# Performance work log

Measured on AMD Instinct MI355X. Metric: run time of the kernel, lower is better.

## Reference

```python
import jax, jax.numpy as jnp
import numpy as np

# Unpooled output spatial size (pooled 128x128 -> unpooled 256x256)
OUT_H, OUT_W = 256, 256


def setup_inputs() -> dict:
    key = jax.random.key(0)
    k1, k2, k3, k4 = jax.random.split(key, 4)
    B, C, OH, OW = 16, 64, 128, 128
    K, P = 4, 4  # kernel_size samples, bilinear taps
    x = jax.random.normal(k1, (B, C, OH, OW), dtype=jnp.float32)
    idx_mask = jax.random.randint(k2, (B, C, OH, OW), 0, K, dtype=jnp.int64)
    sample_map = jax.random.randint(k3, (OH, OW, K, P), 0, OUT_H * OUT_W, dtype=jnp.int64)
    interp_weights = jax.random.uniform(k4, (OH, OW, K, P), dtype=jnp.float32)
    return {"x": x, "idx_mask": idx_mask, "sample_map": sample_map,
            "interp_weights": interp_weights}


def reference(x, idx_mask, sample_map, interp_weights):
    # x: (B,C,OH,OW) pooled values; idx_mask: (B,C,OH,OW) argmax kernel sample in [0,K)
    # sample_map: (OH,OW,K,P) flat indices into OUT_H*OUT_W; interp_weights: (OH,OW,K,P)
    B, C, OH, OW = x.shape
    P = sample_map.shape[-1]
    oh = jnp.arange(OH)[:, None]
    ow = jnp.arange(OW)[None, :]
    # Select, per (b,c,oh,ow), the winning kernel sample's taps and weights -> (B,C,OH,OW,P)
    sel_idx = sample_map[oh, ow, idx_mask]
    sel_w = interp_weights[oh, ow, idx_mask]
    vals = sel_w * x[..., None]  # (B,C,OH,OW,P)
    bb = jnp.arange(B)[:, None, None, None, None]
    cc = jnp.arange(C)[None, :, None, None, None]
    out = jnp.zeros((B, C, OUT_H * OUT_W), dtype=x.dtype)
    out = out.at[bb, cc, sel_idx].add(vals)  # scatter-add (atomic add in CUDA kernel)
    return out.reshape(B, C, OUT_H, OUT_W)
```

## Files before the change

### kernel.cpp

```cpp
#include <hip/hip_runtime.h>
#include <hip/hip_fp16.h>

constexpr int B  = 16;
constexpr int C  = 64;
constexpr int OH = 128;
constexpr int OW = 128;
constexpr int HW = OH * OW;
constexpr int K  = 4;
constexpr int P  = 4;
constexpr int TAPS = HW * K * P;
constexpr int OUT_H = 256;
constexpr int OUT_W = 256;
constexpr int PLANE = OUT_H * OUT_W;
constexpr int NQ = 4;
constexpr int QUARTER = PLANE / NQ;
constexpr int BLOCK = 512;
constexpr size_t TABLE_BYTES = (size_t)HW * K * 16;

constexpr int CHUNK_CAP = 114688;
constexpr size_t WS_SORT_BYTES = ((size_t)PLANE * 5) * 4 + (size_t)CHUNK_CAP * 16;

constexpr int GW = 4;

static __device__ __forceinline__ float h2f(unsigned short u) {
    __half h; __builtin_memcpy(&h, &u, 2); return __half2float(h);
}


__global__ __launch_bounds__(256) void zero_ws_kernel(
    unsigned* __restrict__ counts, uint4* __restrict__ entries)
{
    int r = blockIdx.x * 256 + threadIdx.x;
    if (r < PLANE)     counts[r]  = 0u;
    if (r < CHUNK_CAP) entries[r] = make_uint4(0u, 0u, 0u, 0u);
}

__global__ __launch_bounds__(256) void hist_kernel(
    const int* __restrict__ sm, unsigned* __restrict__ counts)
{
    int r = blockIdx.x * 256 + threadIdx.x;
    if (r < TAPS) atomicAdd(&counts[sm[r]], 1u);
}

__global__ __launch_bounds__(1024) void scan_chunks_kernel(
    const unsigned* __restrict__ counts,
    unsigned* __restrict__ desc, unsigned* __restrict__ cursor)
{
    __shared__ unsigned part[1024];
    const int t = threadIdx.x;
    const int base = t * 64;
    unsigned s = 0;
    for (int j = 0; j < 64; ++j) s += (counts[base + j] + 3u) >> 2;
    part[t] = s;
    __syncthreads();
    for (int st = 1; st < 1024; st <<= 1) {
        unsigned v = (t >= st) ? part[t - st] : 0u;
        __syncthreads();
        part[t] += v;
        __syncthreads();
    }
    unsigned run = part[t] - s;
    for (int j = 0; j < 64; ++j) {
        unsigned c   = counts[base + j];
        unsigned nch = (c + 3u) >> 2;
        desc[base + j]   = run | (nch << 24);
        cursor[base + j] = run * 4u;
        run += nch;
    }
}

__global__ __launch_bounds__(256) void scatter_chunks_kernel(
    const int* __restrict__ sm, const float* __restrict__ iw,
    unsigned* __restrict__ cursor, unsigned* __restrict__ entries_u32)
{
    int r = blockIdx.x * 256 + threadIdx.x;
    if (r >= TAPS) return;
    int o = sm[r];
    unsigned hw = (unsigned)(r >> 4);
    unsigned k  = (unsigned)((r >> 2) & 3);
    __half h = __float2half_rn(iw[r]);
    unsigned short hb; __builtin_memcpy(&hb, &h, 2);
    unsigned ent = (hw << 2) | k | ((unsigned)hb << 16);
    unsigned pos = atomicAdd(&cursor[o], 1u);
    entries_u32[pos] = ent;
}

constexpr int WNB = 32;
__global__ __launch_bounds__(256) void window_sort_kernel(
    const unsigned* __restrict__ desc, uint2* __restrict__ sched)
{
    __shared__ unsigned hist[WNB];
    __shared__ unsigned cur[WNB];
    const int w = blockIdx.x;
    const int t = threadIdx.x;
    const int base = w * 1024;
    if (t < WNB) hist[t] = 0;
    __syncthreads();
    unsigned d[4], nch[4];
    for (int j = 0; j < 4; ++j) {
        d[j] = desc[base + t * 4 + j];
        nch[j] = d[j] >> 24; if (nch[j] > 31u) nch[j] = 31u;
        atomicAdd(&hist[nch[j]], 1u);
    }
    __syncthreads();
    if (t == 0) {
        unsigned run = 0;
        for (int b = 0; b < WNB; ++b) { unsigned v = hist[b]; cur[b] = run; run += v; }
    }
    __syncthreads();
    for (int j = 0; j < 4; ++j) {
        unsigned p = atomicAdd(&cur[nch[j]], 1u);
        sched[base + p] = make_uint2(d[j], (unsigned)(base + t * 4 + j));
    }
}

__global__ __launch_bounds__(1024) void unpool_staged_kernel(
    const float* __restrict__ x,
    const int*   __restrict__ idx_mask,
    const uint2* __restrict__ sched,
    const uint4* __restrict__ entries,
    float* __restrict__ out)
{
    __shared__ unsigned xk[HW];
    __shared__ float    stg[GW * 1024];

    const int bc = blockIdx.x;
    const float4* xp4 = (const float4*)(x + (size_t)bc * HW);
    const int4*   ip4 = (const int4*)(idx_mask + (size_t)bc * HW);
    uint4* xk4 = (uint4*)xk;

    for (int t = threadIdx.x; t < HW / 4; t += 1024) {
        float4 xv = xp4[t];
        int4   kv = ip4[t];
        uint4 o;
        o.x = (__float_as_uint(xv.x) & ~3u) | ((unsigned)kv.x & 3u);
        o.y = (__float_as_uint(xv.y) & ~3u) | ((unsigned)kv.y & 3u);
        o.z = (__float_as_uint(xv.z) & ~3u) | ((unsigned)kv.z & 3u);
        o.w = (__float_as_uint(xv.w) & ~3u) | ((unsigned)kv.w & 3u);
        xk4[t] = o;
    }
    __syncthreads();

    const char* xkb = (const char*)xk;
    const float4* stg4 = (const float4*)stg;
    float4* op4 = (float4*)(out + (size_t)bc * PLANE);

    const int lane = threadIdx.x & 63;
    const int wid  = threadIdx.x >> 6;

    for (int g = 0; g < PLANE / 1024 / GW; ++g) {
        for (int iw2 = 0; iw2 < GW; ++iw2) {
            const int i = g * GW + iw2;
            const int slot = i * 1024 + (((wid + i) & 15) << 6) + lane;
            const uint2 s = sched[slot];
            const unsigned nch = s.x >> 24;
            const uint4* ep = entries + (s.x & 0xffffffu);
            float acc = 0.f;
            for (unsigned j = 0; j < nch; ++j) {
                uint4 ch = ep[j];
                {   unsigned e = ch.x;
                    unsigned u = *(const unsigned*)(xkb + (e & 0xfffcu));
                    float w = (((u ^ e) & 3u) == 0u) ? h2f((unsigned short)(e >> 16)) : 0.f;
                    acc = fmaf(w, __uint_as_float(u & ~3u), acc); }
                {   unsigned e = ch.y;
                    unsigned u = *(const unsigned*)(xkb + (e & 0xfffcu));
                    float w = (((u ^ e) & 3u) == 0u) ? h2f((unsigned short)(e >> 16)) : 0.f;
                    acc = fmaf(w, __uint_as_float(u & ~3u), acc); }
                {   unsigned e = ch.z;
                    unsigned u = *(const unsigned*)(xkb + (e & 0xfffcu));
                    float w = (((u ^ e) & 3u) == 0u) ? h2f((unsigned short)(e >> 16)) : 0.f;
                    acc = fmaf(w, __uint_as_float(u & ~3u), acc); }
                {   unsigned e = ch.w;
                    unsigned u = *(const unsigned*)(xkb + (e & 0xfffcu));
                    float w = (((u ^ e) & 3u) == 0u) ? h2f((unsigned short)(e >> 16)) : 0.f;
                    acc = fmaf(w, __uint_as_float(u & ~3u), acc); }
            }
            stg[iw2 * 1024 + (s.y & 1023)] = acc;
        }
        __syncthreads();
        op4[g * 1024 + threadIdx.x] = stg4[threadIdx.x];
        __syncthreads();
    }
}

__global__ __launch_bounds__(1024) void unpool_chunk_kernel(
    const float* __restrict__ x,
    const int*   __restrict__ idx_mask,
    const unsigned* __restrict__ desc,
    const uint4* __restrict__ entries,
    float* __restrict__ out)
{
    __shared__ unsigned xk[HW];

    const int bc = blockIdx.x;
    const float4* xp4 = (const float4*)(x + (size_t)bc * HW);
    const int4*   ip4 = (const int4*)(idx_mask + (size_t)bc * HW);
    uint4* xk4 = (uint4*)xk;

    for (int t = threadIdx.x; t < HW / 4; t += 1024) {
        float4 xv = xp4[t];
        int4   kv = ip4[t];
        uint4 o;
        o.x = (__float_as_uint(xv.x) & ~3u) | ((unsigned)kv.x & 3u);
        o.y = (__float_as_uint(xv.y) & ~3u) | ((unsigned)kv.y & 3u);
        o.z = (__float_as_uint(xv.z) & ~3u) | ((unsigned)kv.z & 3u);
        o.w = (__float_as_uint(xv.w) & ~3u) | ((unsigned)kv.w & 3u);
        xk4[t] = o;
    }
    __syncthreads();

    const char* xkb = (const char*)xk;
    float* op = out + (size_t)bc * PLANE;

    for (int i = 0; i < PLANE / 1024; ++i) {
        const int o = i * 1024 + threadIdx.x;
        const unsigned d   = desc[o];
        const unsigned nch = d >> 24;
        const uint4* ep = entries + (d & 0xffffffu);
        float acc = 0.f;
        for (unsigned j = 0; j < nch; ++j) {
            uint4 ch = ep[j];
            {   unsigned e = ch.x;
                unsigned u = *(const unsigned*)(xkb + (e & 0xfffcu));
                float w = (((u ^ e) & 3u) == 0u) ? h2f((unsigned short)(e >> 16)) : 0.f;
                acc = fmaf(w, __uint_as_float(u & ~3u), acc); }
            {   unsigned e = ch.y;
                unsigned u = *(const unsigned*)(xkb + (e & 0xfffcu));
                float w = (((u ^ e) & 3u) == 0u) ? h2f((unsigned short)(e >> 16)) : 0.f;
                acc = fmaf(w, __uint_as_float(u & ~3u), acc); }
            {   unsigned e = ch.z;
                unsigned u = *(const unsigned*)(xkb + (e & 0xfffcu));
                float w = (((u ^ e) & 3u) == 0u) ? h2f((unsigned short)(e >> 16)) : 0.f;
                acc = fmaf(w, __uint_as_float(u & ~3u), acc); }
            {   unsigned e = ch.w;
                unsigned u = *(const unsigned*)(xkb + (e & 0xfffcu));
                float w = (((u ^ e) & 3u) == 0u) ? h2f((unsigned short)(e >> 16)) : 0.f;
                acc = fmaf(w, __uint_as_float(u & ~3u), acc); }
        }
        op[o] = acc;
    }
}


static __device__ __forceinline__ uint4 sel4(bool c, uint4 a, uint4 b) {
    return make_uint4(c ? a.x : b.x, c ? a.y : b.y, c ? a.z : b.z, c ? a.w : b.w);
}
static __device__ __forceinline__ float2 u2f2(unsigned u) {
    __half2 h; __builtin_memcpy(&h, &u, 4); return __half22float2(h);
}

__global__ __launch_bounds__(256) void compact_table_kernel(
    const int4* __restrict__ sm, const float4* __restrict__ iw, uint4* __restrict__ ct)
{
    int r = blockIdx.x * blockDim.x + threadIdx.x;
    if (r >= HW * K) return;
    int4   s = sm[r];
    float4 w = iw[r];
    uint4 o;
    o.x = ((unsigned)s.x & 0xffffu) | (((unsigned)s.y & 0xffffu) << 16);
    o.y = ((unsigned)s.z & 0xffffu) | (((unsigned)s.w & 0xffffu) << 16);
    __half2 h01 = __floats2half2_rn(w.x, w.y);
    __half2 h23 = __floats2half2_rn(w.z, w.w);
    __builtin_memcpy(&o.z, &h01, 4);
    __builtin_memcpy(&o.w, &h23, 4);
    ct[r] = o;
}

__global__ __launch_bounds__(BLOCK) void unpool_lds2_kernel(
    const float* __restrict__ x,
    const int*   __restrict__ idx_mask,
    const uint4* __restrict__ ct,
    float* __restrict__ out)
{
    __shared__ float acc[QUARTER];

    const int bc    = blockIdx.x >> 2;
    const int q     = blockIdx.x & 3;
    const int qbase = q * QUARTER;

    float4* acc4 = (float4*)acc;
    for (int t = threadIdx.x; t < QUARTER / 4; t += BLOCK)
        acc4[t] = make_float4(0.f, 0.f, 0.f, 0.f);
    __syncthreads();

    const float* xp = x + (size_t)bc * HW;
    const int*   ip = idx_mask + (size_t)bc * HW;

    for (int hw = threadIdx.x; hw < HW; hw += BLOCK) {
        float xv = xp[hw];
        int   k  = ip[hw];
        const uint4* c = ct + (hw << 2);
        uint4 r0 = c[0], r1 = c[1], r2 = c[2], r3 = c[3];
        uint4 rl = sel4(k & 1, r1, r0);
        uint4 rh = sel4(k & 1, r3, r2);
        uint4 r  = sel4(k & 2, rh, rl);

        int i0 = r.x & 0xffff, i1 = (int)(r.x >> 16);
        int i2 = r.y & 0xffff, i3 = (int)(r.y >> 16);
        float2 w01 = u2f2(r.z);
        float2 w23 = u2f2(r.w);

        int a;
        a = i0 - qbase; if ((unsigned)a < (unsigned)QUARTER) atomicAdd(&acc[a], w01.x * xv);
        a = i1 - qbase; if ((unsigned)a < (unsigned)QUARTER) atomicAdd(&acc[a], w01.y * xv);
        a = i2 - qbase; if ((unsigned)a < (unsigned)QUARTER) atomicAdd(&acc[a], w23.x * xv);
        a = i3 - qbase; if ((unsigned)a < (unsigned)QUARTER) atomicAdd(&acc[a], w23.y * xv);
    }
    __syncthreads();

    float4* op4 = (float4*)(out + (size_t)bc * PLANE + qbase);
    for (int t = threadIdx.x; t < QUARTER / 4; t += BLOCK)
        op4[t] = acc4[t];
}

__global__ __launch_bounds__(256) void unpool_lds_fallback_kernel(
    const float* __restrict__ x,
    const int*   __restrict__ idx_mask,
    const int4*  __restrict__ sample_map,
    const float4* __restrict__ interp_w,
    float* __restrict__ out)
{
    __shared__ float acc[QUARTER];
    const int bc    = blockIdx.x >> 2;
    const int q     = blockIdx.x & 3;
    const int qbase = q * QUARTER;
    float4* acc4 = (float4*)acc;
    for (int t = threadIdx.x; t < QUARTER / 4; t += 256)
        acc4[t] = make_float4(0.f, 0.f, 0.f, 0.f);
    __syncthreads();
    const float* xp = x + (size_t)bc * HW;
    const int*   ip = idx_mask + (size_t)bc * HW;
    for (int hw = threadIdx.x; hw < HW; hw += 256) {
        float xv = xp[hw];
        int   k  = ip[hw];
        int row = hw * K + k;
        int4   sel = sample_map[row];
        float4 w   = interp_w[row];
        int a;
        a = sel.x - qbase; if ((unsigned)a < (unsigned)QUARTER) atomicAdd(&acc[a], w.x * xv);
        a = sel.y - qbase; if ((unsigned)a < (unsigned)QUARTER) atomicAdd(&acc[a], w.y * xv);
        a = sel.z - qbase; if ((unsigned)a < (unsigned)QUARTER) atomicAdd(&acc[a], w.z * xv);
        a = sel.w - qbase; if ((unsigned)a < (unsigned)QUARTER) atomicAdd(&acc[a], w.w * xv);
    }
    __syncthreads();
    float4* op4 = (float4*)(out + (size_t)bc * PLANE + qbase);
    for (int t = threadIdx.x; t < QUARTER / 4; t += 256)
        op4[t] = acc4[t];
}

extern "C" void kernel_launch(void* const* d_in, const int* in_sizes, int n_in,
                              void* d_out, int out_size, void* d_ws, size_t ws_size,
                              hipStream_t stream) {
    const float*  x          = (const float*)d_in[0];
    const int*    idx_mask   = (const int*)d_in[1];
    const int*    sample_map = (const int*)d_in[2];
    const float*  interp_w   = (const float*)d_in[3];
    float* out = (float*)d_out;

    if (ws_size >= WS_SORT_BYTES) {
        unsigned* desc    = (unsigned*)d_ws;
        unsigned* cursor  = desc + PLANE;
        unsigned* counts  = cursor + PLANE;
        uint2*    sched   = (uint2*)(counts + PLANE);
        uint4*    entries = (uint4*)(counts + PLANE + 2 * PLANE);

        zero_ws_kernel<<<(CHUNK_CAP + 255) / 256, 256, 0, stream>>>(counts, entries);
        hist_kernel<<<TAPS / 256, 256, 0, stream>>>(sample_map, counts);
        scan_chunks_kernel<<<1, 1024, 0, stream>>>(counts, desc, cursor);
        scatter_chunks_kernel<<<TAPS / 256, 256, 0, stream>>>(
            sample_map, interp_w, cursor, (unsigned*)entries);
        window_sort_kernel<<<PLANE / 1024, 256, 0, stream>>>(desc, sched);
        unpool_staged_kernel<<<B * C, 1024, 0, stream>>>(x, idx_mask, sched, entries, out);
        if (hipGetLastError() != hipSuccess) {
            unpool_chunk_kernel<<<B * C, 1024, 0, stream>>>(x, idx_mask, desc, entries, out);
        }
    } else if (ws_size >= TABLE_BYTES) {
        uint4* ct = (uint4*)d_ws;
        compact_table_kernel<<<(HW * K + 255) / 256, 256, 0, stream>>>(
            (const int4*)sample_map, (const float4*)interp_w, ct);
        unpool_lds2_kernel<<<B * C * NQ, BLOCK, 0, stream>>>(
            x, idx_mask, ct, out);
    } else {
        unpool_lds_fallback_kernel<<<B * C * NQ, 256, 0, stream>>>(
            x, idx_mask, (const int4*)sample_map, (const float4*)interp_w, out);
    }
}
```

Baseline: 546.6 us.

## Interleave per-group tap entries for coalesced wavefront loads in unpool gather

Adds a new workspace path that groups output pixels into 64-wide groups sorted by chunk count, then lays out their tap entries interleaved by lane so each wavefront reads contiguous uint4s per step. A group scan computes per-group base offsets and the scatter kernel writes entries into the strided interleaved layout. The gather kernel prefetches the next chunk and stages results in LDS for coalesced output stores. It needs a larger workspace and pads every group to its longest member's chunk count, which adds wasted entries. The old chunk fallback kernel is removed.

```diff
diff --git a/kernel.cpp b/kernel.cpp
--- a/kernel.cpp
+++ b/kernel.cpp
@@ -17,13 +17,172 @@
 constexpr int BLOCK = 512;
 constexpr size_t TABLE_BYTES = (size_t)HW * K * 16;
 
+constexpr int GW = 4;
+constexpr int NGROUP = PLANE / 64;
+
+constexpr int E2CAP = 229376;
+constexpr size_t WS_V2_BYTES = ((size_t)PLANE * 4 + 2048) * 4 + (size_t)E2CAP * 16;
+
 constexpr int CHUNK_CAP = 114688;
 constexpr size_t WS_SORT_BYTES = ((size_t)PLANE * 5) * 4 + (size_t)CHUNK_CAP * 16;
 
-constexpr int GW = 4;
-
 static __device__ __forceinline__ float h2f(unsigned short u) {
     __half h; __builtin_memcpy(&h, &u, 2); return __half2float(h);
+}
+
+
+__global__ __launch_bounds__(256) void hist_kernel(
+    const int* __restrict__ sm, unsigned* __restrict__ counts)
+{
+    int r = blockIdx.x * 256 + threadIdx.x;
+    if (r < TAPS) atomicAdd(&counts[sm[r]], 1u);
+}
+
+
+__global__ __launch_bounds__(256) void zero_v2_kernel(
+    unsigned* __restrict__ counts, unsigned* __restrict__ cursor,
+    uint4* __restrict__ entries2)
+{
+    int r = blockIdx.x * 256 + threadIdx.x;
+    if (r < PLANE) { counts[r] = 0u; cursor[r] = 0u; }
+    if (r < E2CAP) entries2[r] = make_uint4(0u, 0u, 0u, 0u);
+}
+
+constexpr int WNB = 32;
+__global__ __launch_bounds__(256) void window_sort_v2_kernel(
+    const unsigned* __restrict__ counts, unsigned* __restrict__ sched)
+{
+    __shared__ unsigned hist[WNB];
+    __shared__ unsigned cur[WNB];
+    const int w = blockIdx.x;
+    const int t = threadIdx.x;
+    const int base = w * 1024;
+    if (t < WNB) hist[t] = 0;
+    __syncthreads();
+    unsigned nch[4];
+    for (int j = 0; j < 4; ++j) {
+        unsigned c = counts[base + t * 4 + j];
+        nch[j] = (c + 3u) >> 2; if (nch[j] > 31u) nch[j] = 31u;
+        atomicAdd(&hist[nch[j]], 1u);
+    }
+    __syncthreads();
+    if (t == 0) {
+        unsigned run = 0;
+        for (int b = 0; b < WNB; ++b) { unsigned v = hist[b]; cur[b] = run; run += v; }
+    }
+    __syncthreads();
+    for (int j = 0; j < 4; ++j) {
+        unsigned p = atomicAdd(&cur[nch[j]], 1u);
+        sched[base + p] = (unsigned)(base + t * 4 + j);
+    }
+}
+
+__global__ __launch_bounds__(1024) void group_scan_kernel(
+    const unsigned* __restrict__ counts, const unsigned* __restrict__ sched,
+    unsigned* __restrict__ gdesc, unsigned* __restrict__ wbase)
+{
+    __shared__ unsigned part[NGROUP];
+    const int g = threadIdx.x;
+    unsigned olast = sched[g * 64 + 63];
+    unsigned M = (counts[olast] + 3u) >> 2;
+    part[g] = M;
+    __syncthreads();
+    for (int st = 1; st < NGROUP; st <<= 1) {
+        unsigned v = (g >= st) ? part[g - st] : 0u;
+        __syncthreads();
+        part[g] += v;
+        __syncthreads();
+    }
+    unsigned rowbase = part[g] - M;
+    gdesc[g] = (rowbase << 6) | (M << 24);
+    unsigned wb = (rowbase << 6) * 4u;
+    for (int l = 0; l < 64; ++l)
+        wbase[sched[g * 64 + l]] = wb + (unsigned)(l * 4);
+}
+
+__global__ __launch_bounds__(256) void scatter_v2_kernel(
+    const int* __restrict__ sm, const float* __restrict__ iw,
+    unsigned* __restrict__ cursor, const unsigned* __restrict__ wbase,
+    unsigned* __restrict__ entries2_u32)
+{
+    int r = blockIdx.x * 256 + threadIdx.x;
+    if (r >= TAPS) return;
+    int o = sm[r];
+    unsigned hw = (unsigned)(r >> 4);
+    unsigned k  = (unsigned)((r >> 2) & 3);
+    __half h = __float2half_rn(iw[r]);
+    unsigned short hb; __builtin_memcpy(&hb, &h, 2);
+    unsigned ent = (hw << 2) | k | ((unsigned)hb << 16);
+    unsigned idx = atomicAdd(&cursor[o], 1u);
+    entries2_u32[wbase[o] + ((idx >> 2) << 8) + (idx & 3u)] = ent;
+}
+
+__global__ __launch_bounds__(1024) void unpool_grouped_kernel(
+    const float* __restrict__ x,
+    const int*   __restrict__ idx_mask,
+    const unsigned* __restrict__ sched,
+    const unsigned* __restrict__ gdesc,
+    const uint4* __restrict__ entries2,
+    float* __restrict__ out)
+{
+    __shared__ unsigned xk[HW];
+    __shared__ float    stg[GW * 1024];
+
+    const int bc = blockIdx.x;
+    const float4* xp4 = (const float4*)(x + (size_t)bc * HW);
+    const int4*   ip4 = (const int4*)(idx_mask + (size_t)bc * HW);
+    uint4* xk4 = (uint4*)xk;
+
+    for (int t = threadIdx.x; t < HW / 4; t += 1024) {
+        float4 xv = xp4[t];
+        int4   kv = ip4[t];
+        uint4 o;
+        o.x = (__float_as_uint(xv.x) & ~3u) | ((unsigned)kv.x & 3u);
+        o.y = (__float_as_uint(xv.y) & ~3u) | ((unsigned)kv.y & 3u);
+        o.z = (__float_as_uint(xv.z) & ~3u) | ((unsigned)kv.z & 3u);
+        o.w = (__float_as_uint(xv.w) & ~3u) | ((unsigned)kv.w & 3u);
+        xk4[t] = o;
+    }
+    __syncthreads();
+
+    const char* xkb = (const char*)xk;
+    const float4* stg4 = (const float4*)stg;
+    float4* op4 = (float4*)(out + (size_t)bc * PLANE);
+
+    const int lane = threadIdx.x & 63;
+    const int wid  = threadIdx.x >> 6;
+
+#define PROC1(E) { unsigned e = (E); \
+    unsigned u = *(const unsigned*)(xkb + (e & 0xfffcu)); \
+    float w = (((u ^ e) & 3u) == 0u) ? h2f((unsigned short)(e >> 16)) : 0.f; \
+    acc = fmaf(w, __uint_as_float(u), acc); }
+
+    for (int gq = 0; gq < PLANE / 1024 / GW; ++gq) {
+        for (int iw2 = 0; iw2 < GW; ++iw2) {
+            const int i = gq * GW + iw2;
+            const int s = (wid + i) & 15;
+            const int g = i * 16 + s;
+            const unsigned gd = gdesc[g];
+            const unsigned M  = gd >> 24;
+            const uint4* ep = entries2 + (gd & 0xffffffu) + lane;
+            float acc = 0.f;
+            if (M) {
+                uint4 ch = ep[0];
+                for (unsigned j = 1; j < M; ++j) {
+                    uint4 nx = ep[j << 6];
+                    PROC1(ch.x) PROC1(ch.y) PROC1(ch.z) PROC1(ch.w)
+                    ch = nx;
+                }
+                PROC1(ch.x) PROC1(ch.y) PROC1(ch.z) PROC1(ch.w)
+            }
+            const unsigned oid = sched[g * 64 + lane];
+            stg[iw2 * 1024 + (oid & 1023u)] = acc;
+        }
+        __syncthreads();
+        op4[gq * 1024 + threadIdx.x] = stg4[threadIdx.x];
+        __syncthreads();
+    }
+#undef PROC1
 }
 
 
@@ -33,13 +192,6 @@
     int r = blockIdx.x * 256 + threadIdx.x;
     if (r < PLANE)     counts[r]  = 0u;
     if (r < CHUNK_CAP) entries[r] = make_uint4(0u, 0u, 0u, 0u);
-}
-
-__global__ __launch_bounds__(256) void hist_kernel(
-    const int* __restrict__ sm, unsigned* __restrict__ counts)
-{
-    int r = blockIdx.x * 256 + threadIdx.x;
-    if (r < TAPS) atomicAdd(&counts[sm[r]], 1u);
 }
 
 __global__ __launch_bounds__(1024) void scan_chunks_kernel(
@@ -85,7 +237,6 @@
     entries_u32[pos] = ent;
 }
 
-constexpr int WNB = 32;
 __global__ __launch_bounds__(256) void window_sort_kernel(
     const unsigned* __restrict__ desc, uint2* __restrict__ sched)
 {
@@ -183,64 +334,6 @@
     }
 }
 
-__global__ __launch_bounds__(1024) void unpool_chunk_kernel(
-    const float* __restrict__ x,
-    const int*   __restrict__ idx_mask,
-    const unsigned* __restrict__ desc,
-    const uint4* __restrict__ entries,
-    float* __restrict__ out)
-{
-    __shared__ unsigned xk[HW];
-
-    const int bc = blockIdx.x;
-    const float4* xp4 = (const float4*)(x + (size_t)bc * HW);
-    const int4*   ip4 = (const int4*)(idx_mask + (size_t)bc * HW);
-    uint4* xk4 = (uint4*)xk;
-
-    for (int t = threadIdx.x; t < HW / 4; t += 1024) {
-        float4 xv = xp4[t];
-        int4   kv = ip4[t];
-        uint4 o;
-        o.x = (__float_as_uint(xv.x) & ~3u) | ((unsigned)kv.x & 3u);
-        o.y = (__float_as_uint(xv.y) & ~3u) | ((unsigned)kv.y & 3u);
-        o.z = (__float_as_uint(xv.z) & ~3u) | ((unsigned)kv.z & 3u);
-        o.w = (__float_as_uint(xv.w) & ~3u) | ((unsigned)kv.w & 3u);
-        xk4[t] = o;
-    }
-    __syncthreads();
-
-    const char* xkb = (const char*)xk;
-    float* op = out + (size_t)bc * PLANE;
-
-    for (int i = 0; i < PLANE / 1024; ++i) {
-        const int o = i * 1024 + threadIdx.x;
-        const unsigned d   = desc[o];
-        const unsigned nch = d >> 24;
-        const uint4* ep = entries + (d & 0xffffffu);
-        float acc = 0.f;
-        for (unsigned j = 0; j < nch; ++j) {
-            uint4 ch = ep[j];
-            {   unsigned e = ch.x;
-                unsigned u = *(const unsigned*)(xkb + (e & 0xfffcu));
-                float w = (((u ^ e) & 3u) == 0u) ? h2f((unsigned short)(e >> 16)) : 0.f;
-                acc = fmaf(w, __uint_as_float(u & ~3u), acc); }
-            {   unsigned e = ch.y;
-                unsigned u = *(const unsigned*)(xkb + (e & 0xfffcu));
-                float w = (((u ^ e) & 3u) == 0u) ? h2f((unsigned short)(e >> 16)) : 0.f;
-                acc = fmaf(w, __uint_as_float(u & ~3u), acc); }
-            {   unsigned e = ch.z;
-                unsigned u = *(const unsigned*)(xkb + (e & 0xfffcu));
-                float w = (((u ^ e) & 3u) == 0u) ? h2f((unsigned short)(e >> 16)) : 0.f;
-                acc = fmaf(w, __uint_as_float(u & ~3u), acc); }
-            {   unsigned e = ch.w;
-                unsigned u = *(const unsigned*)(xkb + (e & 0xfffcu));
-                float w = (((u ^ e) & 3u) == 0u) ? h2f((unsigned short)(e >> 16)) : 0.f;
-                acc = fmaf(w, __uint_as_float(u & ~3u), acc); }
-        }
-        op[o] = acc;
-    }
-}
-
 
 static __device__ __forceinline__ uint4 sel4(bool c, uint4 a, uint4 b) {
     return make_uint4(c ? a.x : b.x, c ? a.y : b.y, c ? a.z : b.z, c ? a.w : b.w);
@@ -357,7 +450,23 @@
     const float*  interp_w   = (const float*)d_in[3];
     float* out = (float*)d_out;
 
-    if (ws_size >= WS_SORT_BYTES) {
+    if (ws_size >= WS_V2_BYTES) {
+        unsigned* counts   = (unsigned*)d_ws;
+        unsigned* cursor   = counts + PLANE;
+        unsigned* sched    = cursor + PLANE;
+        unsigned* wbase    = sched + PLANE;
+        unsigned* gdesc    = wbase + PLANE;
+        uint4*    entries2 = (uint4*)(gdesc + 2048);
+
+        zero_v2_kernel<<<(E2CAP + 255) / 256, 256, 0, stream>>>(counts, cursor, entries2);
+        hist_kernel<<<TAPS / 256, 256, 0, stream>>>(sample_map, counts);
+        window_sort_v2_kernel<<<PLANE / 1024, 256, 0, stream>>>(counts, sched);
+        group_scan_kernel<<<1, NGROUP, 0, stream>>>(counts, sched, gdesc, wbase);
+        scatter_v2_kernel<<<TAPS / 256, 256, 0, stream>>>(
+            sample_map, interp_w, cursor, wbase, (unsigned*)entries2);
+        unpool_grouped_kernel<<<B * C, 1024, 0, stream>>>(
+            x, idx_mask, sched, gdesc, entries2, out);
+    } else if (ws_size >= WS_SORT_BYTES) {
         unsigned* desc    = (unsigned*)d_ws;
         unsigned* cursor  = desc + PLANE;
         unsigned* counts  = cursor + PLANE;
@@ -371,9 +480,6 @@
             sample_map, interp_w, cursor, (unsigned*)entries);
         window_sort_kernel<<<PLANE / 1024, 256, 0, stream>>>(desc, sched);
         unpool_staged_kernel<<<B * C, 1024, 0, stream>>>(x, idx_mask, sched, entries, out);
-        if (hipGetLastError() != hipSuccess) {
-            unpool_chunk_kernel<<<B * C, 1024, 0, stream>>>(x, idx_mask, desc, entries, out);
-        }
     } else if (ws_size >= TABLE_BYTES) {
         uint4* ct = (uint4*)d_ws;
         compact_table_kernel<<<(HW * K + 255) / 256, 256, 0, stream>>>(
```

Result: no change. 541.2 us (-1.0%).
